# Optimization experiments

Measured on AMD Instinct MI355X. Metric: run time of the kernel, lower is better.

Reference implementation:

```python
import jax, jax.numpy as jnp
import numpy as np

HEAD_NUM = 8
EMB = 256
HEAD_SIZE = EMB // HEAD_NUM
POS_LEN = 128
ROPE_BASE = 100.0
LN_EPS = 1e-5
SOFTPICK_EPS = 1e-6


def _rope_tables():
    inv_freq = 1.0 / ROPE_BASE ** (jnp.arange(0, HEAD_SIZE, 2, dtype=jnp.float32) / HEAD_SIZE)
    t = jnp.arange(POS_LEN, dtype=jnp.float32)
    freqs = jnp.einsum('i,j->ij', t, inv_freq)          # [W, hs/2]
    freqs = jnp.concatenate([freqs, freqs], axis=-1)     # [W, hs]
    return jnp.sin(freqs), jnp.cos(freqs)


def _apply_rope(e, sin, cos):
    # e: [..., W, hs]; sin/cos: [W, hs]
    h = HEAD_SIZE // 2
    rot = jnp.concatenate([-e[..., h:], e[..., :h]], axis=-1)
    return e * cos + rot * sin


def _layernorm(x, g, b):
    mu = jnp.mean(x, axis=-1, keepdims=True)
    var = jnp.mean(jnp.square(x - mu), axis=-1, keepdims=True)
    return (x - mu) * jax.lax.rsqrt(var + LN_EPS) * g + b


def _softpick(x):
    m = jnp.max(x, axis=-1, keepdims=True)
    e = jnp.exp(x - m) - jnp.exp(-m)
    return jax.nn.relu(e) / (jnp.sum(jnp.abs(e), axis=-1, keepdims=True) + SOFTPICK_EPS)


def setup_inputs() -> dict:
    key = jax.random.key(0)
    ks = jax.random.split(key, 12)
    B, C, H, W = 4, EMB, 256, 128
    hn, hs = HEAD_NUM, HEAD_SIZE
    s = 0.02
    return {
        'left': jax.random.normal(ks[0], (B, C, H, W), jnp.float32),
        'right': jax.random.normal(ks[1], (B, C, H, W), jnp.float32),
        'qw': jax.random.normal(ks[2], (hn, hs, hs), jnp.float32) * s,   # grouped 1x1 conv weights
        'kw': jax.random.normal(ks[3], (hn, hs, hs), jnp.float32) * s,
        'vw': jax.random.normal(ks[4], (hn, hs, hs), jnp.float32) * s,
        'proj_w': jax.random.normal(ks[5], (C, C), jnp.float32) * s,
        'proj_b': jnp.zeros((C,), jnp.float32),
        'ln1_g': jnp.ones((C,), jnp.float32),
        'ln1_b': jnp.zeros((C,), jnp.float32),
        'ln2_g': jnp.ones((C,), jnp.float32),
        'ln2_b': jnp.zeros((C,), jnp.float32),
        'w1': jax.random.normal(ks[6], (C, 4 * C), jnp.float32) * s,
        'b1': jnp.zeros((4 * C,), jnp.float32),
        'w2': jax.random.normal(ks[7], (4 * C, C), jnp.float32) * s,
        'b2': jnp.zeros((C,), jnp.float32),
    }


def reference(left, right, qw, kw, vw, proj_w, proj_b,
              ln1_g, ln1_b, ln2_g, ln2_b, w1, b1, w2, b2):
    B, C, H, W = left.shape
    hn, hs = HEAD_NUM, HEAD_SIZE
    scale = hs ** -0.5
    sin, cos = _rope_tables()  # [W, hs]

    def grouped_proj(x, w):
        # grouped 1x1 conv -> per-head matmul; out [B, H, hn, W, hs]
        xr = x.reshape(B, hn, hs, H, W)
        return jnp.einsum('bgihw,goi->bhgwo', xr, w)

    q = _apply_rope(grouped_proj(left, qw), sin, cos)
    k = _apply_rope(grouped_proj(right, kw), sin, cos)
    v = grouped_proj(right, vw)

    att = _softpick(jnp.einsum('bhgqd,bhgkd->bhgqk', q, k) * scale)  # [B,H,hn,W,W]
    out = jnp.einsum('bhgqk,bhgkd->bhqgd', att, v).reshape(B, H, W, C)

    x1 = _layernorm(out @ proj_w + proj_b + jnp.transpose(left, (0, 2, 3, 1)), ln1_g, ln1_b)
    ffn = jax.nn.gelu(x1 @ w1 + b1, approximate=False) @ w2 + b2
    return _layernorm(ffn + x1, ln2_g, ln2_b)
```

## Files before the change

kernel.cpp:

```cpp
#include <hip/hip_runtime.h>
#include <hip/hip_bf16.h>

#define DEV __device__ __forceinline__

typedef __attribute__((ext_vector_type(8))) short bf16x8_t;
typedef __attribute__((ext_vector_type(4))) float f32x4_t;

constexpr int cB = 4, cC = 256, cH = 256, cW = 128, cHN = 8, cHS = 32;
constexpr int cM = cB * cH * cW;

DEV float bfu(unsigned int b16) { union { unsigned int u; float f; } v; v.u = b16 << 16; return v.f; }
DEV unsigned short f2bb(float f) { union { __hip_bfloat16 h; unsigned short u; } v; v.h = __float2bfloat16(f); return v.u; }
DEV unsigned int pk2(float a, float b) { return (unsigned)f2bb(a) | ((unsigned)f2bb(b) << 16); }

#define GLOAD_LDS16(g, l) \
  __builtin_amdgcn_global_load_lds((const __attribute__((address_space(1))) void*)(g), \
                                   (__attribute__((address_space(3))) void*)(l), 16, 0, 0)

DEV float gelu_fast(float v) {
  float ax = fabsf(v) * 0.7071067811865475f;
  float t = __builtin_amdgcn_rcpf(1.0f + 0.3275911f * ax);
  float poly = ((((1.061405429f * t - 1.453152027f) * t + 1.421413741f) * t
                 - 0.284496736f) * t + 0.254829592f) * t;
  float e = __expf(-ax * ax);
  float erfv = 1.0f - poly * e;
  float phi = 0.5f + 0.5f * copysignf(erfv, v);
  return v * phi;
}

__global__ __launch_bounds__(256) void transpose_bf16(const float* __restrict__ src,
                                                      __hip_bfloat16* __restrict__ dst,
                                                      int R, int Ccol) {
  int idx = blockIdx.x * 256 + threadIdx.x;
  if (idx < R * Ccol) {
    int r = idx / Ccol, c = idx - r * Ccol;
    dst[c * R + r] = __float2bfloat16(src[idx]);
  }
}

__global__ __launch_bounds__(256) void transpose_perm_fp8(const float* __restrict__ src,
                                                          unsigned char* __restrict__ dst,
                                                          int R, int Ccol) {
  int idx = blockIdx.x * 256 + threadIdx.x;
  if (idx < R * Ccol) {
    int r = idx / Ccol, c = idx - r * Ccol;
    int pk = (r & ~63) | ((r & 15) << 2) | ((r >> 4) & 3);
    int u = __builtin_amdgcn_cvt_pk_fp8_f32(src[idx] * 64.0f, 0.0f, 0, false);
    dst[(size_t)c * R + pk] = (unsigned char)(u & 0xff);
  }
}

__global__ __launch_bounds__(256) void rope_init(float2* __restrict__ tab) {
  int i = blockIdx.x * 256 + threadIdx.x;
  int w = i >> 4, c = i & 15;
  float inv = expf((float)c * -0.28782313662425572f);
  float ang = (float)w * inv;
  tab[i] = make_float2(sinf(ang), cosf(ang));
}

constexpr int XL_OFF = 0, XR_OFF = 10240, WQ_OFF = 20480, WK_OFF = 23040, WV_OFF = 25600;
constexpr int QS_OFF = 28160, KS_OFF = 38400, VT_OFF = 0, P_OFF = 10240;
constexpr int SMEM_BYTES = 48640;

__global__ __launch_bounds__(256) void attn_mfma(
    const float* __restrict__ left, const float* __restrict__ right,
    const float* __restrict__ qw, const float* __restrict__ kw, const float* __restrict__ vw,
    const float2* __restrict__ rope,
    __hip_bfloat16* __restrict__ att_out)
{
  __shared__ __align__(16) char smem[SMEM_BYTES];

  const int t = threadIdx.x;
  const int g = blockIdx.x & 7;
  const int h = (blockIdx.x >> 3) & 255;
  const int b = blockIdx.x >> 11;
  const size_t HW = (size_t)cH * cW;

  {
    const float* lb = left  + ((size_t)(b * cC + g * cHS) * cH + h) * cW;
    const float* rb = right + ((size_t)(b * cC + g * cHS) * cH + h) * cW;
    int w = t & 127, ih = (t >> 7) * 16;
    unsigned short* xlrow = (unsigned short*)(smem + XL_OFF) + w * 40 + ih;
    unsigned short* xrrow = (unsigned short*)(smem + XR_OFF) + w * 40 + ih;
#pragma unroll
    for (int i = 0; i < 16; i += 2) {
      float a0 = lb[(size_t)(ih + i) * HW + w], a1 = lb[(size_t)(ih + i + 1) * HW + w];
      *(unsigned int*)(xlrow + i) = pk2(a0, a1);
      float c0 = rb[(size_t)(ih + i) * HW + w], c1 = rb[(size_t)(ih + i + 1) * HW + w];
      *(unsigned int*)(xrrow + i) = pk2(c0, c1);
    }
    int o = t >> 3, i0 = (t & 7) * 4;
    {
      float4 v4 = *(const float4*)(qw + g * 1024 + t * 4);
      unsigned short* dst = (unsigned short*)(smem + WQ_OFF) + o * 40 + i0;
      *(unsigned int*)(dst) = pk2(v4.x, v4.y); *(unsigned int*)(dst + 2) = pk2(v4.z, v4.w);
    }
    {
      float4 v4 = *(const float4*)(kw + g * 1024 + t * 4);
      unsigned short* dst = (unsigned short*)(smem + WK_OFF) + o * 40 + i0;
      *(unsigned int*)(dst) = pk2(v4.x, v4.y); *(unsigned int*)(dst + 2) = pk2(v4.z, v4.w);
    }
    {
      float4 v4 = *(const float4*)(vw + g * 1024 + t * 4);
      unsigned short* dst = (unsigned short*)(smem + WV_OFF) + o * 40 + i0;
      *(unsigned int*)(dst) = pk2(v4.x, v4.y); *(unsigned int*)(dst + 2) = pk2(v4.z, v4.w);
    }
  }
  __syncthreads();

  const int lane = t & 63, wid = t >> 6;
  const int c = lane & 15, q4 = lane >> 4;
  const int wbase = wid * 32;
  const f32x4_t zero = {0.f, 0.f, 0.f, 0.f};

  bf16x8_t a_xl[2], a_xr[2];
#pragma unroll
  for (int sub = 0; sub < 2; ++sub) {
    a_xl[sub] = *(const bf16x8_t*)(smem + XL_OFF + (wbase + sub * 16 + c) * 80 + q4 * 16);
    a_xr[sub] = *(const bf16x8_t*)(smem + XR_OFF + (wbase + sub * 16 + c) * 80 + q4 * 16);
  }
  f32x4_t qacc[2][2], kacc[2][2];
#pragma unroll
  for (int ot = 0; ot < 2; ++ot) {
    bf16x8_t bq = *(const bf16x8_t*)(smem + WQ_OFF + (ot * 16 + c) * 80 + q4 * 16);
    bf16x8_t bk = *(const bf16x8_t*)(smem + WK_OFF + (ot * 16 + c) * 80 + q4 * 16);
#pragma unroll
    for (int sub = 0; sub < 2; ++sub) {
      qacc[sub][ot] = __builtin_amdgcn_mfma_f32_16x16x32_bf16(a_xl[sub], bq, zero, 0, 0, 0);
      kacc[sub][ot] = __builtin_amdgcn_mfma_f32_16x16x32_bf16(a_xr[sub], bk, zero, 0, 0, 0);
    }
  }
  {
    const float scale = 0.17677669529663687f;
    unsigned short* qsp = (unsigned short*)(smem + QS_OFF);
    unsigned short* ksp = (unsigned short*)(smem + KS_OFF);
#pragma unroll
    for (int sub = 0; sub < 2; ++sub)
#pragma unroll
      for (int r = 0; r < 4; ++r) {
        int w = wbase + sub * 16 + q4 * 4 + r;
        float2 sc = rope[w * 16 + c];
        float sn = sc.x, cs = sc.y;
        float q0 = qacc[sub][0][r], q1 = qacc[sub][1][r];
        qsp[w * 40 + c]      = f2bb((q0 * cs - q1 * sn) * scale);
        qsp[w * 40 + c + 16] = f2bb((q1 * cs + q0 * sn) * scale);
        float k0 = kacc[sub][0][r], k1 = kacc[sub][1][r];
        ksp[w * 40 + c]      = f2bb(k0 * cs - k1 * sn);
        ksp[w * 40 + c + 16] = f2bb(k1 * cs + k0 * sn);
      }
  }
  __syncthreads();

  {
    f32x4_t vacc[2][2];
#pragma unroll
    for (int dt = 0; dt < 2; ++dt) {
      bf16x8_t awv = *(const bf16x8_t*)(smem + WV_OFF + (dt * 16 + c) * 80 + q4 * 16);
#pragma unroll
      for (int sub = 0; sub < 2; ++sub)
        vacc[dt][sub] = __builtin_amdgcn_mfma_f32_16x16x32_bf16(awv, a_xr[sub], zero, 0, 0, 0);
    }
    unsigned short* vtp = (unsigned short*)(smem + VT_OFF);
#pragma unroll
    for (int dt = 0; dt < 2; ++dt)
#pragma unroll
      for (int r = 0; r < 4; ++r) {
        int d = dt * 16 + q4 * 4 + r;
        *(unsigned int*)(vtp + d * 136 + c * 8 + wid * 2) = pk2(vacc[dt][0][r], vacc[dt][1][r]);
      }
  }

  bf16x8_t aq0 = *(const bf16x8_t*)(smem + QS_OFF + (wbase + c) * 80 + q4 * 16);
  bf16x8_t aq1 = *(const bf16x8_t*)(smem + QS_OFF + (wbase + 16 + c) * 80 + q4 * 16);
  f32x4_t sac[2][8];
#pragma unroll
  for (int kt = 0; kt < 8; ++kt) {
    bf16x8_t bk = *(const bf16x8_t*)(smem + KS_OFF + (kt * 16 + c) * 80 + q4 * 16);
    sac[0][kt] = __builtin_amdgcn_mfma_f32_16x16x32_bf16(aq0, bk, zero, 0, 0, 0);
    sac[1][kt] = __builtin_amdgcn_mfma_f32_16x16x32_bf16(aq1, bk, zero, 0, 0, 0);
  }

  float dinv_[2][4];
#pragma unroll
  for (int sub = 0; sub < 2; ++sub)
#pragma unroll
    for (int r = 0; r < 4; ++r) {
      float m = sac[sub][0][r];
#pragma unroll
      for (int kt = 1; kt < 8; ++kt) m = fmaxf(m, sac[sub][kt][r]);
      m = fmaxf(m, __shfl_xor(m, 1));
      m = fmaxf(m, __shfl_xor(m, 2));
      m = fmaxf(m, __shfl_xor(m, 4));
      m = fmaxf(m, __shfl_xor(m, 8));
      float em = __expf(-m);
      float ss = 0.f;
#pragma unroll
      for (int kt = 0; kt < 8; ++kt) {
        float e = __expf(sac[sub][kt][r] - m) - em;
        sac[sub][kt][r] = fmaxf(e, 0.f);
        ss += fabsf(e);
      }
      ss += __shfl_xor(ss, 1);
      ss += __shfl_xor(ss, 2);
      ss += __shfl_xor(ss, 4);
      ss += __shfl_xor(ss, 8);
      dinv_[sub][r] = 1.0f / (ss + 1e-6f);
    }
  __syncthreads();

  {
    unsigned short* pp = (unsigned short*)(smem + P_OFF);
#pragma unroll
    for (int sub = 0; sub < 2; ++sub)
#pragma unroll
      for (int r = 0; r < 4; ++r) {
        int w = wbase + sub * 16 + q4 * 4 + r;
        float dv = dinv_[sub][r];
        uint4 u;
        u.x = pk2(sac[sub][0][r] * dv, sac[sub][1][r] * dv);
        u.y = pk2(sac[sub][2][r] * dv, sac[sub][3][r] * dv);
        u.z = pk2(sac[sub][4][r] * dv, sac[sub][5][r] * dv);
        u.w = pk2(sac[sub][6][r] * dv, sac[sub][7][r] * dv);
        *(uint4*)(pp + w * 136 + c * 8) = u;
      }
  }
  f32x4_t oacc[2][2] = {{zero, zero}, {zero, zero}};
#pragma unroll
  for (int ks = 0; ks < 4; ++ks) {
    bf16x8_t ap0 = *(const bf16x8_t*)(smem + P_OFF + (wbase + c) * 272 + ks * 64 + q4 * 16);
    bf16x8_t ap1 = *(const bf16x8_t*)(smem + P_OFF + (wbase + 16 + c) * 272 + ks * 64 + q4 * 16);
    bf16x8_t bv0 = *(const bf16x8_t*)(smem + VT_OFF + (c) * 272 + ks * 64 + q4 * 16);
    bf16x8_t bv1 = *(const bf16x8_t*)(smem + VT_OFF + (16 + c) * 272 + ks * 64 + q4 * 16);
    oacc[0][0] = __builtin_amdgcn_mfma_f32_16x16x32_bf16(ap0, bv0, oacc[0][0], 0, 0, 0);
    oacc[0][1] = __builtin_amdgcn_mfma_f32_16x16x32_bf16(ap0, bv1, oacc[0][1], 0, 0, 0);
    oacc[1][0] = __builtin_amdgcn_mfma_f32_16x16x32_bf16(ap1, bv0, oacc[1][0], 0, 0, 0);
    oacc[1][1] = __builtin_amdgcn_mfma_f32_16x16x32_bf16(ap1, bv1, oacc[1][1], 0, 0, 0);
  }
  {
    __hip_bfloat16* ob = att_out + ((size_t)(b * cH + h) * cW) * cC + g * cHS;
#pragma unroll
    for (int sub = 0; sub < 2; ++sub)
#pragma unroll
      for (int dt = 0; dt < 2; ++dt)
#pragma unroll
        for (int r = 0; r < 4; ++r) {
          int w = wbase + sub * 16 + q4 * 4 + r;
          ob[(size_t)w * cC + dt * 16 + c] = __float2bfloat16(oacc[sub][dt][r]);
        }
  }
}

__global__ __launch_bounds__(256) void ffn1_gemm(
    const __hip_bfloat16* __restrict__ A, const __hip_bfloat16* __restrict__ Bt,
    const float* __restrict__ bias, unsigned char* __restrict__ outb)
{
  constexpr int K = 256, N = 1024;
  __shared__ __align__(16) char smem[49152];
  const int t = threadIdx.x;
  const int id = blockIdx.x;
  const int slot = id >> 3;
  const int by = (id & 7) * 128 + (slot >> 3);
  const int bx = slot & 7;
  const int m0 = by * 128, n0 = bx * 128;
  const int lane = t & 63, wid = t >> 6;
  const int r16 = lane & 15, kq = lane >> 4;
  const int wr = (wid >> 1) * 64, wc = (wid & 1) * 64;

  f32x4_t acc[4][4];
#pragma unroll
  for (int fi = 0; fi < 4; ++fi)
#pragma unroll
    for (int fj = 0; fj < 4; ++fj) acc[fi][fj] = {0.f, 0.f, 0.f, 0.f};

  auto stage = [&](int buf, int k0) {
    char* As = smem + buf * 16384;
    char* Bs = As + 8192;
#pragma unroll
    for (int i = 0; i < 2; ++i) {
      int chunk = i * 4 + wid;
      int row = chunk * 16 + (lane >> 2);
      int sw = (((lane & 3) ^ ((row >> 1) & 3))) * 8;
      GLOAD_LDS16(A  + (size_t)(m0 + row) * K + k0 + sw, As + chunk * 1024);
      GLOAD_LDS16(Bt + (size_t)(n0 + row) * K + k0 + sw, Bs + chunk * 1024);
    }
  };

  constexpr int NK = K >> 5;
  stage(0, 0);
  stage(1, 32);
  for (int tt = 0; tt < NK; ++tt) {
    if (tt + 2 < NK) {
      stage((tt + 2) % 3, (tt + 2) << 5);
      asm volatile("s_waitcnt vmcnt(8)" ::: "memory");
    } else if (tt + 1 < NK) {
      asm volatile("s_waitcnt vmcnt(4)" ::: "memory");
    } else {
      asm volatile("s_waitcnt vmcnt(0)" ::: "memory");
    }
    __builtin_amdgcn_s_barrier();
    __builtin_amdgcn_sched_barrier(0);
    char* As = smem + (tt % 3) * 16384;
    char* Bs = As + 8192;
    bf16x8_t af[4], bf[4];
#pragma unroll
    for (int fi = 0; fi < 4; ++fi) {
      int rr = wr + fi * 16 + r16;
      af[fi] = *(const bf16x8_t*)(As + rr * 64 + ((kq ^ ((rr >> 1) & 3)) * 16));
    }
#pragma unroll
    for (int fj = 0; fj < 4; ++fj) {
      int rr = wc + fj * 16 + r16;
      bf[fj] = *(const bf16x8_t*)(Bs + rr * 64 + ((kq ^ ((rr >> 1) & 3)) * 16));
    }
#pragma unroll
    for (int fi = 0; fi < 4; ++fi)
#pragma unroll
      for (int fj = 0; fj < 4; ++fj)
        acc[fi][fj] = __builtin_amdgcn_mfma_f32_16x16x32_bf16(af[fi], bf[fj], acc[fi][fj], 0, 0, 0);
    __builtin_amdgcn_sched_barrier(0);
    __builtin_amdgcn_s_barrier();
  }

  float bv[4];
#pragma unroll
  for (int fj = 0; fj < 4; ++fj) bv[fj] = bias[n0 + wc + fj * 16 + r16];
  unsigned char* obase = outb + (size_t)(m0 + wr + kq * 4) * N + n0 + wc + r16 * 4;
#pragma unroll
  for (int fi = 0; fi < 4; ++fi)
#pragma unroll
    for (int r = 0; r < 4; ++r) {
      float v0 = gelu_fast(acc[fi][0][r] + bv[0]) * 64.0f;
      float v1 = gelu_fast(acc[fi][1][r] + bv[1]) * 64.0f;
      float v2 = gelu_fast(acc[fi][2][r] + bv[2]) * 64.0f;
      float v3 = gelu_fast(acc[fi][3][r] + bv[3]) * 64.0f;
      int u = __builtin_amdgcn_cvt_pk_fp8_f32(v0, v1, 0, false);
      u = __builtin_amdgcn_cvt_pk_fp8_f32(v2, v3, u, true);
      *(unsigned int*)(obase + (size_t)(fi * 16 + r) * N) = (unsigned)u;
    }
}

__global__ __launch_bounds__(256, 2) void proj_gemm_ln(
    const __hip_bfloat16* __restrict__ A, const __hip_bfloat16* __restrict__ Bt,
    const float* __restrict__ bias, const float* __restrict__ leftres,
    const float* __restrict__ g, const float* __restrict__ be,
    __hip_bfloat16* __restrict__ outp)
{
  constexpr int KK = 256;
  __shared__ __align__(16) char smem[73728];
  const int t = threadIdx.x, lane = t & 63, wid = t >> 6;
  const int c = lane & 15, q4 = lane >> 4;
  const int m0 = blockIdx.x * 128;
  const int wr = wid * 32;
  const f32x4_t zero = {0.f, 0.f, 0.f, 0.f};

  f32x4_t acc[2][16];
#pragma unroll
  for (int fi = 0; fi < 2; ++fi)
#pragma unroll
    for (int fj = 0; fj < 16; ++fj) acc[fi][fj] = zero;

  auto stage = [&](int buf, int k0) {
    char* As = smem + buf * 24576;
    char* Bs = As + 8192;
#pragma unroll
    for (int i = 0; i < 2; ++i) {
      int chunk = (wid * 2 + i);
      int row = chunk * 16 + (lane >> 2);
      int sw = (((lane & 3) ^ ((row >> 1) & 3))) * 8;
      GLOAD_LDS16(A + (size_t)(m0 + row) * KK + k0 + sw, As + chunk * 1024);
    }
#pragma unroll
    for (int i = 0; i < 4; ++i) {
      int chunk = (wid * 4 + i);
      int row = chunk * 16 + (lane >> 2);
      int sw = (((lane & 3) ^ ((row >> 1) & 3))) * 8;
      GLOAD_LDS16(Bt + (size_t)row * KK + k0 + sw, Bs + chunk * 1024);
    }
  };

  constexpr int NK = KK >> 5;
  stage(0, 0);
  stage(1, 32);
  for (int tt = 0; tt < NK; ++tt) {
    if (tt + 2 < NK) {
      stage((tt + 2) % 3, (tt + 2) << 5);
      asm volatile("s_waitcnt vmcnt(12)" ::: "memory");
    } else if (tt + 1 < NK) {
      asm volatile("s_waitcnt vmcnt(6)" ::: "memory");
    } else {
      asm volatile("s_waitcnt vmcnt(0)" ::: "memory");
    }
    __builtin_amdgcn_s_barrier();
    __builtin_amdgcn_sched_barrier(0);
    char* As = smem + (tt % 3) * 24576;
    char* Bs = As + 8192;
    int ra0 = wr + c, ra1 = wr + 16 + c;
    bf16x8_t af0 = *(const bf16x8_t*)(As + ra0 * 64 + ((q4 ^ ((ra0 >> 1) & 3)) * 16));
    bf16x8_t af1 = *(const bf16x8_t*)(As + ra1 * 64 + ((q4 ^ ((ra1 >> 1) & 3)) * 16));
#pragma unroll
    for (int fj = 0; fj < 16; ++fj) {
      int rb = fj * 16 + c;
      bf16x8_t bf = *(const bf16x8_t*)(Bs + rb * 64 + ((q4 ^ ((rb >> 1) & 3)) * 16));
      acc[0][fj] = __builtin_amdgcn_mfma_f32_16x16x32_bf16(af0, bf, acc[0][fj], 0, 0, 0);
      acc[1][fj] = __builtin_amdgcn_mfma_f32_16x16x32_bf16(af1, bf, acc[1][fj], 0, 0, 0);
    }
    __builtin_amdgcn_sched_barrier(0);
    __builtin_amdgcn_s_barrier();
  }

  {
    const int b_ = m0 >> 15, h_ = (m0 >> 7) & 255;
#pragma unroll
    for (int fj = 0; fj < 16; ++fj) {
      int n = fj * 16 + c;
      float bv = bias[n];
#pragma unroll
      for (int fi = 0; fi < 2; ++fi) {
        int w0 = wr + fi * 16 + q4 * 4;
        float4 lr = *(const float4*)(leftres + (((size_t)b_ * 256 + n) * 256 + h_) * 128 + w0);
        float la[4] = {lr.x, lr.y, lr.z, lr.w};
#pragma unroll
        for (int r = 0; r < 4; ++r) acc[fi][fj][r] += bv + la[r];
      }
    }
  }

  float mu[2][4], rs[2][4];
#pragma unroll
  for (int fi = 0; fi < 2; ++fi)
#pragma unroll
    for (int r = 0; r < 4; ++r) {
      float s = 0.f;
#pragma unroll
      for (int fj = 0; fj < 16; ++fj) s += acc[fi][fj][r];
      s += __shfl_xor(s, 1); s += __shfl_xor(s, 2); s += __shfl_xor(s, 4); s += __shfl_xor(s, 8);
      float m_ = s * (1.0f / 256.0f);
      float sq = 0.f;
#pragma unroll
      for (int fj = 0; fj < 16; ++fj) { float d = acc[fi][fj][r] - m_; sq += d * d; }
      sq += __shfl_xor(sq, 1); sq += __shfl_xor(sq, 2); sq += __shfl_xor(sq, 4); sq += __shfl_xor(sq, 8);
      mu[fi][r] = m_;
      rs[fi][r] = rsqrtf(sq * (1.0f / 256.0f) + 1e-5f);
    }
#pragma unroll
  for (int fj = 0; fj < 16; ++fj) {
    int n = fj * 16 + c;
    float gv = g[n], bev = be[n];
#pragma unroll
    for (int fi = 0; fi < 2; ++fi)
#pragma unroll
      for (int r = 0; r < 4; ++r) {
        int row = wr + fi * 16 + q4 * 4 + r;
        outp[(size_t)(m0 + row) * 256 + n] =
            __float2bfloat16((acc[fi][fj][r] - mu[fi][r]) * rs[fi][r] * gv + bev);
      }
  }
}

__global__ __launch_bounds__(256, 2) void ffn2_ln(
    const unsigned char* __restrict__ A, const unsigned char* __restrict__ Bt,
    const float* __restrict__ bias, const __hip_bfloat16* __restrict__ resbf,
    const float* __restrict__ g, const float* __restrict__ be,
    float* __restrict__ outp)
{
  constexpr int KK = 1024;
  __shared__ __align__(16) char smem[73728];
  const int t = threadIdx.x, lane = t & 63, wid = t >> 6;
  const int c = lane & 15, q4 = lane >> 4;
  const int m0 = blockIdx.x * 128;
  const int wr = wid * 32;
  const f32x4_t zero = {0.f, 0.f, 0.f, 0.f};

  f32x4_t acc[2][16];
#pragma unroll
  for (int fi = 0; fi < 2; ++fi)
#pragma unroll
    for (int fj = 0; fj < 16; ++fj) acc[fi][fj] = zero;

  auto stage = [&](int buf, int k0) {
    char* As = smem + buf * 24576;
    char* Bs = As + 8192;
#pragma unroll
    for (int i = 0; i < 2; ++i) {
      int chunk = (wid * 2 + i);
      int row = chunk * 16 + (lane >> 2);
      int sw = (((lane & 3) ^ ((row >> 1) & 3))) * 16;
      GLOAD_LDS16(A + (size_t)(m0 + row) * KK + k0 + sw, As + chunk * 1024);
    }
#pragma unroll
    for (int i = 0; i < 4; ++i) {
      int chunk = (wid * 4 + i);
      int row = chunk * 16 + (lane >> 2);
      int sw = (((lane & 3) ^ ((row >> 1) & 3))) * 16;
      GLOAD_LDS16(Bt + (size_t)row * KK + k0 + sw, Bs + chunk * 1024);
    }
  };

  constexpr int NK = 16;
  stage(0, 0);
  stage(1, 64);
  const int sl = (c >> 1) & 3;
  const int koff0 = ((((q4 >> 1)) ^ sl) << 4) | ((q4 & 1) << 3);
  const int koff1 = (((2 | (q4 >> 1)) ^ sl) << 4) | ((q4 & 1) << 3);
  for (int tt = 0; tt < NK; ++tt) {
    if (tt + 2 < NK) {
      stage((tt + 2) % 3, (tt + 2) << 6);
      asm volatile("s_waitcnt vmcnt(12)" ::: "memory");
    } else if (tt + 1 < NK) {
      asm volatile("s_waitcnt vmcnt(6)" ::: "memory");
    } else {
      asm volatile("s_waitcnt vmcnt(0)" ::: "memory");
    }
    __builtin_amdgcn_s_barrier();
    __builtin_amdgcn_sched_barrier(0);
    char* As = smem + (tt % 3) * 24576;
    char* Bs = As + 8192;
    const char* arow0 = As + (wr + c) * 64;
    const char* arow1 = As + (wr + 16 + c) * 64;
    long a00 = *(const long*)(arow0 + koff0);
    long a01 = *(const long*)(arow0 + koff1);
    long a10 = *(const long*)(arow1 + koff0);
    long a11 = *(const long*)(arow1 + koff1);
#pragma unroll
    for (int fj = 0; fj < 16; ++fj) {
      const char* brow = Bs + (fj * 16 + c) * 64;
      long b0 = *(const long*)(brow + koff0);
      long b1 = *(const long*)(brow + koff1);
      acc[0][fj] = __builtin_amdgcn_mfma_f32_16x16x32_fp8_fp8(a00, b0, acc[0][fj], 0, 0, 0);
      acc[0][fj] = __builtin_amdgcn_mfma_f32_16x16x32_fp8_fp8(a01, b1, acc[0][fj], 0, 0, 0);
      acc[1][fj] = __builtin_amdgcn_mfma_f32_16x16x32_fp8_fp8(a10, b0, acc[1][fj], 0, 0, 0);
      acc[1][fj] = __builtin_amdgcn_mfma_f32_16x16x32_fp8_fp8(a11, b1, acc[1][fj], 0, 0, 0);
    }
    __builtin_amdgcn_sched_barrier(0);
    __builtin_amdgcn_s_barrier();
  }

#pragma unroll
  for (int fj = 0; fj < 16; ++fj) {
    int n = fj * 16 + c;
    float bv = bias[n];
#pragma unroll
    for (int fi = 0; fi < 2; ++fi)
#pragma unroll
      for (int r = 0; r < 4; ++r) {
        int row = wr + fi * 16 + q4 * 4 + r;
        acc[fi][fj][r] = acc[fi][fj][r] * 0.000244140625f + bv +
                         __bfloat162float(resbf[(size_t)(m0 + row) * 256 + n]);
      }
  }

  float mu[2][4], rs[2][4];
#pragma unroll
  for (int fi = 0; fi < 2; ++fi)
#pragma unroll
    for (int r = 0; r < 4; ++r) {
      float s = 0.f;
#pragma unroll
      for (int fj = 0; fj < 16; ++fj) s += acc[fi][fj][r];
      s += __shfl_xor(s, 1); s += __shfl_xor(s, 2); s += __shfl_xor(s, 4); s += __shfl_xor(s, 8);
      float m_ = s * (1.0f / 256.0f);
      float sq = 0.f;
#pragma unroll
      for (int fj = 0; fj < 16; ++fj) { float d = acc[fi][fj][r] - m_; sq += d * d; }
      sq += __shfl_xor(sq, 1); sq += __shfl_xor(sq, 2); sq += __shfl_xor(sq, 4); sq += __shfl_xor(sq, 8);
      mu[fi][r] = m_;
      rs[fi][r] = rsqrtf(sq * (1.0f / 256.0f) + 1e-5f);
    }
#pragma unroll
  for (int fj = 0; fj < 16; ++fj) {
    int n = fj * 16 + c;
    float gv = g[n], bev = be[n];
#pragma unroll
    for (int fi = 0; fi < 2; ++fi)
#pragma unroll
      for (int r = 0; r < 4; ++r) {
        int row = wr + fi * 16 + q4 * 4 + r;
        outp[(size_t)(m0 + row) * 256 + n] =
            (acc[fi][fj][r] - mu[fi][r]) * rs[fi][r] * gv + bev;
      }
  }
}

extern "C" void kernel_launch(void* const* d_in, const int* in_sizes, int n_in,
                              void* d_out, int out_size, void* d_ws, size_t ws_size,
                              hipStream_t stream) {
  const float* left   = (const float*)d_in[0];
  const float* right  = (const float*)d_in[1];
  const float* qw     = (const float*)d_in[2];
  const float* kw     = (const float*)d_in[3];
  const float* vw     = (const float*)d_in[4];
  const float* proj_w = (const float*)d_in[5];
  const float* proj_b = (const float*)d_in[6];
  const float* ln1_g  = (const float*)d_in[7];
  const float* ln1_b  = (const float*)d_in[8];
  const float* ln2_g  = (const float*)d_in[9];
  const float* ln2_b  = (const float*)d_in[10];
  const float* w1     = (const float*)d_in[11];
  const float* b1     = (const float*)d_in[12];
  const float* w2     = (const float*)d_in[13];
  const float* b2     = (const float*)d_in[14];

  char* ws = (char*)d_ws;
  __hip_bfloat16* att_out = (__hip_bfloat16*)ws;
  __hip_bfloat16* x1      = (__hip_bfloat16*)(ws + 67108864);
  unsigned char*  hidden  = (unsigned char*)(ws + 134217728);
  float2*         rope    = (float2*)(ws + 134217728);
  __hip_bfloat16* pwT     = (__hip_bfloat16*)(ws + 402653184);
  __hip_bfloat16* w1T     = pwT + 65536;
  unsigned char*  w2T     = (unsigned char*)(w1T + 262144);

  transpose_bf16<<<256, 256, 0, stream>>>(proj_w, pwT, 256, 256);
  transpose_bf16<<<1024, 256, 0, stream>>>(w1, w1T, 256, 1024);
  transpose_perm_fp8<<<1024, 256, 0, stream>>>(w2, w2T, 1024, 256);
  rope_init<<<8, 256, 0, stream>>>(rope);

  attn_mfma<<<cB * cH * cHN, 256, 0, stream>>>(left, right, qw, kw, vw, rope, att_out);

  proj_gemm_ln<<<cM / 128, 256, 0, stream>>>(att_out, pwT, proj_b, left, ln1_g, ln1_b, x1);
  ffn1_gemm<<<8192, 256, 0, stream>>>(x1, w1T, b1, hidden);
  ffn2_ln<<<cM / 128, 256, 0, stream>>>(hidden, w2T, b2, x1, ln2_g, ln2_b, (float*)d_out);
}
```

Before: 406.4 us.

## Widen FFN1 GEMM tile to 128x256 with 16-byte FP8 stores and matching w2 permutation

```diff
diff --git a/kernel.cpp b/kernel.cpp
--- a/kernel.cpp
+++ b/kernel.cpp
@@ -44,7 +44,7 @@
   int idx = blockIdx.x * 256 + threadIdx.x;
   if (idx < R * Ccol) {
     int r = idx / Ccol, c = idx - r * Ccol;
-    int pk = (r & ~63) | ((r & 15) << 2) | ((r >> 4) & 3);
+    int pk = (r & ~255) | ((r & 15) << 4) | ((r >> 4) & 15);
     int u = __builtin_amdgcn_cvt_pk_fp8_f32(src[idx] * 64.0f, 0.0f, 0, false);
     dst[(size_t)c * R + pk] = (unsigned char)(u & 0xff);
   }
@@ -248,95 +248,6 @@
           ob[(size_t)w * cC + dt * 16 + c] = __float2bfloat16(oacc[sub][dt][r]);
         }
   }
-}
-
-__global__ __launch_bounds__(256) void ffn1_gemm(
-    const __hip_bfloat16* __restrict__ A, const __hip_bfloat16* __restrict__ Bt,
-    const float* __restrict__ bias, unsigned char* __restrict__ outb)
-{
-  constexpr int K = 256, N = 1024;
-  __shared__ __align__(16) char smem[49152];
-  const int t = threadIdx.x;
-  const int id = blockIdx.x;
-  const int slot = id >> 3;
-  const int by = (id & 7) * 128 + (slot >> 3);
-  const int bx = slot & 7;
-  const int m0 = by * 128, n0 = bx * 128;
-  const int lane = t & 63, wid = t >> 6;
-  const int r16 = lane & 15, kq = lane >> 4;
-  const int wr = (wid >> 1) * 64, wc = (wid & 1) * 64;
-
-  f32x4_t acc[4][4];
-#pragma unroll
-  for (int fi = 0; fi < 4; ++fi)
-#pragma unroll
-    for (int fj = 0; fj < 4; ++fj) acc[fi][fj] = {0.f, 0.f, 0.f, 0.f};
-
-  auto stage = [&](int buf, int k0) {
-    char* As = smem + buf * 16384;
-    char* Bs = As + 8192;
-#pragma unroll
-    for (int i = 0; i < 2; ++i) {
-      int chunk = i * 4 + wid;
-      int row = chunk * 16 + (lane >> 2);
-      int sw = (((lane & 3) ^ ((row >> 1) & 3))) * 8;
-      GLOAD_LDS16(A  + (size_t)(m0 + row) * K + k0 + sw, As + chunk * 1024);
-      GLOAD_LDS16(Bt + (size_t)(n0 + row) * K + k0 + sw, Bs + chunk * 1024);
-    }
-  };
-
-  constexpr int NK = K >> 5;
-  stage(0, 0);
-  stage(1, 32);
-  for (int tt = 0; tt < NK; ++tt) {
-    if (tt + 2 < NK) {
-      stage((tt + 2) % 3, (tt + 2) << 5);
-      asm volatile("s_waitcnt vmcnt(8)" ::: "memory");
-    } else if (tt + 1 < NK) {
-      asm volatile("s_waitcnt vmcnt(4)" ::: "memory");
-    } else {
-      asm volatile("s_waitcnt vmcnt(0)" ::: "memory");
-    }
-    __builtin_amdgcn_s_barrier();
-    __builtin_amdgcn_sched_barrier(0);
-    char* As = smem + (tt % 3) * 16384;
-    char* Bs = As + 8192;
-    bf16x8_t af[4], bf[4];
-#pragma unroll
-    for (int fi = 0; fi < 4; ++fi) {
-      int rr = wr + fi * 16 + r16;
-      af[fi] = *(const bf16x8_t*)(As + rr * 64 + ((kq ^ ((rr >> 1) & 3)) * 16));
-    }
-#pragma unroll
-    for (int fj = 0; fj < 4; ++fj) {
-      int rr = wc + fj * 16 + r16;
-      bf[fj] = *(const bf16x8_t*)(Bs + rr * 64 + ((kq ^ ((rr >> 1) & 3)) * 16));
-    }
-#pragma unroll
-    for (int fi = 0; fi < 4; ++fi)
-#pragma unroll
-      for (int fj = 0; fj < 4; ++fj)
-        acc[fi][fj] = __builtin_amdgcn_mfma_f32_16x16x32_bf16(af[fi], bf[fj], acc[fi][fj], 0, 0, 0);
-    __builtin_amdgcn_sched_barrier(0);
-    __builtin_amdgcn_s_barrier();
-  }
-
-  float bv[4];
-#pragma unroll
-  for (int fj = 0; fj < 4; ++fj) bv[fj] = bias[n0 + wc + fj * 16 + r16];
-  unsigned char* obase = outb + (size_t)(m0 + wr + kq * 4) * N + n0 + wc + r16 * 4;
-#pragma unroll
-  for (int fi = 0; fi < 4; ++fi)
-#pragma unroll
-    for (int r = 0; r < 4; ++r) {
-      float v0 = gelu_fast(acc[fi][0][r] + bv[0]) * 64.0f;
-      float v1 = gelu_fast(acc[fi][1][r] + bv[1]) * 64.0f;
-      float v2 = gelu_fast(acc[fi][2][r] + bv[2]) * 64.0f;
-      float v3 = gelu_fast(acc[fi][3][r] + bv[3]) * 64.0f;
-      int u = __builtin_amdgcn_cvt_pk_fp8_f32(v0, v1, 0, false);
-      u = __builtin_amdgcn_cvt_pk_fp8_f32(v2, v3, u, true);
-      *(unsigned int*)(obase + (size_t)(fi * 16 + r) * N) = (unsigned)u;
-    }
 }
 
 __global__ __launch_bounds__(256, 2) void proj_gemm_ln(
@@ -455,6 +366,100 @@
             __float2bfloat16((acc[fi][fj][r] - mu[fi][r]) * rs[fi][r] * gv + bev);
       }
   }
+}
+
+__global__ __launch_bounds__(256, 2) void ffn1_wide(
+    const __hip_bfloat16* __restrict__ A, const __hip_bfloat16* __restrict__ Bt,
+    const float* __restrict__ bias, unsigned char* __restrict__ outb)
+{
+  constexpr int KK = 256, N = 1024;
+  __shared__ __align__(16) char smem[73728];
+  const int t = threadIdx.x, lane = t & 63, wid = t >> 6;
+  const int c = lane & 15, q4 = lane >> 4;
+  const int mb = blockIdx.x & 1023, nc = blockIdx.x >> 10;
+  const int m0 = mb * 128, n0 = nc * 256;
+  const int wr = wid * 32;
+  const f32x4_t zero = {0.f, 0.f, 0.f, 0.f};
+
+  f32x4_t acc[2][16];
+#pragma unroll
+  for (int fi = 0; fi < 2; ++fi)
+#pragma unroll
+    for (int fj = 0; fj < 16; ++fj) acc[fi][fj] = zero;
+
+  const __hip_bfloat16* Bbase = Bt + (size_t)n0 * KK;
+
+  auto stage = [&](int buf, int k0) {
+    char* As = smem + buf * 24576;
+    char* Bs = As + 8192;
+#pragma unroll
+    for (int i = 0; i < 2; ++i) {
+      int chunk = (wid * 2 + i);
+      int row = chunk * 16 + (lane >> 2);
+      int sw = (((lane & 3) ^ ((row >> 1) & 3))) * 8;
+      GLOAD_LDS16(A + (size_t)(m0 + row) * KK + k0 + sw, As + chunk * 1024);
+    }
+#pragma unroll
+    for (int i = 0; i < 4; ++i) {
+      int chunk = (wid * 4 + i);
+      int row = chunk * 16 + (lane >> 2);
+      int sw = (((lane & 3) ^ ((row >> 1) & 3))) * 8;
+      GLOAD_LDS16(Bbase + (size_t)row * KK + k0 + sw, Bs + chunk * 1024);
+    }
+  };
+
+  constexpr int NK = KK >> 5;
+  stage(0, 0);
+  stage(1, 32);
+  for (int tt = 0; tt < NK; ++tt) {
+    if (tt + 2 < NK) {
+      stage((tt + 2) % 3, (tt + 2) << 5);
+      asm volatile("s_waitcnt vmcnt(12)" ::: "memory");
+    } else if (tt + 1 < NK) {
+      asm volatile("s_waitcnt vmcnt(6)" ::: "memory");
+    } else {
+      asm volatile("s_waitcnt vmcnt(0)" ::: "memory");
+    }
+    __builtin_amdgcn_s_barrier();
+    __builtin_amdgcn_sched_barrier(0);
+    char* As = smem + (tt % 3) * 24576;
+    char* Bs = As + 8192;
+    int ra0 = wr + c, ra1 = wr + 16 + c;
+    bf16x8_t af0 = *(const bf16x8_t*)(As + ra0 * 64 + ((q4 ^ ((ra0 >> 1) & 3)) * 16));
+    bf16x8_t af1 = *(const bf16x8_t*)(As + ra1 * 64 + ((q4 ^ ((ra1 >> 1) & 3)) * 16));
+#pragma unroll
+    for (int fj = 0; fj < 16; ++fj) {
+      int rb = fj * 16 + c;
+      bf16x8_t bf = *(const bf16x8_t*)(Bs + rb * 64 + ((q4 ^ ((rb >> 1) & 3)) * 16));
+      acc[0][fj] = __builtin_amdgcn_mfma_f32_16x16x32_bf16(af0, bf, acc[0][fj], 0, 0, 0);
+      acc[1][fj] = __builtin_amdgcn_mfma_f32_16x16x32_bf16(af1, bf, acc[1][fj], 0, 0, 0);
+    }
+    __builtin_amdgcn_sched_barrier(0);
+    __builtin_amdgcn_s_barrier();
+  }
+
+  float bv[16];
+#pragma unroll
+  for (int fj = 0; fj < 16; ++fj) bv[fj] = bias[n0 + fj * 16 + c];
+  unsigned char* obase = outb + (size_t)(m0 + wr + q4 * 4) * N + n0 + c * 16;
+#pragma unroll
+  for (int fi = 0; fi < 2; ++fi)
+#pragma unroll
+    for (int r = 0; r < 4; ++r) {
+      uint4 u;
+      unsigned int* up = (unsigned int*)&u;
+#pragma unroll
+      for (int p = 0; p < 4; ++p) {
+        float v0 = gelu_fast(acc[fi][4 * p + 0][r] + bv[4 * p + 0]) * 64.0f;
+        float v1 = gelu_fast(acc[fi][4 * p + 1][r] + bv[4 * p + 1]) * 64.0f;
+        float v2 = gelu_fast(acc[fi][4 * p + 2][r] + bv[4 * p + 2]) * 64.0f;
+        float v3 = gelu_fast(acc[fi][4 * p + 3][r] + bv[4 * p + 3]) * 64.0f;
+        int w = __builtin_amdgcn_cvt_pk_fp8_f32(v0, v1, 0, false);
+        w = __builtin_amdgcn_cvt_pk_fp8_f32(v2, v3, w, true);
+        up[p] = (unsigned)w;
+      }
+      *(uint4*)(obase + (size_t)(fi * 16 + r) * N) = u;
+    }
 }
 
 __global__ __launch_bounds__(256, 2) void ffn2_ln(
@@ -604,7 +609,7 @@
   __hip_bfloat16* att_out = (__hip_bfloat16*)ws;
   __hip_bfloat16* x1      = (__hip_bfloat16*)(ws + 67108864);
   unsigned char*  hidden  = (unsigned char*)(ws + 134217728);
-  float2*         rope    = (float2*)(ws + 134217728);
+  float2*         rope    = (float2*)(ws + 301989888);
   __hip_bfloat16* pwT     = (__hip_bfloat16*)(ws + 402653184);
   __hip_bfloat16* w1T     = pwT + 65536;
   unsigned char*  w2T     = (unsigned char*)(w1T + 262144);
@@ -617,6 +622,6 @@
   attn_mfma<<<cB * cH * cHN, 256, 0, stream>>>(left, right, qw, kw, vw, rope, att_out);
 
   proj_gemm_ln<<<cM / 128, 256, 0, stream>>>(att_out, pwT, proj_b, left, ln1_g, ln1_b, x1);
-  ffn1_gemm<<<8192, 256, 0, stream>>>(x1, w1T, b1, hidden);
+  ffn1_wide<<<4096, 256, 0, stream>>>(x1, w1T, b1, hidden);
   ffn2_ln<<<cM / 128, 256, 0, stream>>>(hidden, w2T, b2, x1, ln2_g, ln2_b, (float*)d_out);
 }
```

Result: no change. 411.7 us (+1.3%).

## Load attention inputs straight to registers and use FP8 for PV matmul

Applied to the files above, without the earlier changes.

```diff
diff --git a/kernel.cpp b/kernel.cpp
--- a/kernel.cpp
+++ b/kernel.cpp
@@ -58,11 +58,11 @@
   tab[i] = make_float2(sinf(ang), cosf(ang));
 }
 
-constexpr int XL_OFF = 0, XR_OFF = 10240, WQ_OFF = 20480, WK_OFF = 23040, WV_OFF = 25600;
-constexpr int QS_OFF = 28160, KS_OFF = 38400, VT_OFF = 0, P_OFF = 10240;
-constexpr int SMEM_BYTES = 48640;
-
-__global__ __launch_bounds__(256) void attn_mfma(
+constexpr int WQ_OFF = 0, WK_OFF = 2560, WV_OFF = 5120, QS_OFF = 7680, KS_OFF = 17920;
+constexpr int VT_OFF = 28160, P_OFF = 0;
+constexpr int SMEM_BYTES = 32512;
+
+__global__ __launch_bounds__(256, 4) void attn_mfma(
     const float* __restrict__ left, const float* __restrict__ right,
     const float* __restrict__ qw, const float* __restrict__ kw, const float* __restrict__ vw,
     const float2* __restrict__ rope,
@@ -76,19 +76,35 @@
   const int b = blockIdx.x >> 11;
   const size_t HW = (size_t)cH * cW;
 
+  const int lane = t & 63, wid = t >> 6;
+  const int c = lane & 15, q4 = lane >> 4;
+  const int wbase = wid * 32;
+  const f32x4_t zero = {0.f, 0.f, 0.f, 0.f};
+
+  const float* lb = left  + ((size_t)(b * cC + g * cHS) * cH + h) * cW;
+  const float* rb = right + ((size_t)(b * cC + g * cHS) * cH + h) * cW;
+
+  bf16x8_t a_xl[2], a_xr[2];
+#pragma unroll
+  for (int sub = 0; sub < 2; ++sub) {
+    int w = wbase + sub * 16 + c;
+    float xl[8], xr[8];
+#pragma unroll
+    for (int e = 0; e < 8; ++e) {
+      xl[e] = lb[(size_t)(q4 * 8 + e) * HW + w];
+      xr[e] = rb[(size_t)(q4 * 8 + e) * HW + w];
+    }
+    union { bf16x8_t v; unsigned int u[4]; } ul, ur;
+#pragma unroll
+    for (int p = 0; p < 4; ++p) {
+      ul.u[p] = pk2(xl[2 * p], xl[2 * p + 1]);
+      ur.u[p] = pk2(xr[2 * p], xr[2 * p + 1]);
+    }
+    a_xl[sub] = ul.v;
+    a_xr[sub] = ur.v;
+  }
+
   {
-    const float* lb = left  + ((size_t)(b * cC + g * cHS) * cH + h) * cW;
-    const float* rb = right + ((size_t)(b * cC + g * cHS) * cH + h) * cW;
-    int w = t & 127, ih = (t >> 7) * 16;
-    unsigned short* xlrow = (unsigned short*)(smem + XL_OFF) + w * 40 + ih;
-    unsigned short* xrrow = (unsigned short*)(smem + XR_OFF) + w * 40 + ih;
-#pragma unroll
-    for (int i = 0; i < 16; i += 2) {
-      float a0 = lb[(size_t)(ih + i) * HW + w], a1 = lb[(size_t)(ih + i + 1) * HW + w];
-      *(unsigned int*)(xlrow + i) = pk2(a0, a1);
-      float c0 = rb[(size_t)(ih + i) * HW + w], c1 = rb[(size_t)(ih + i + 1) * HW + w];
-      *(unsigned int*)(xrrow + i) = pk2(c0, c1);
-    }
     int o = t >> 3, i0 = (t & 7) * 4;
     {
       float4 v4 = *(const float4*)(qw + g * 1024 + t * 4);
@@ -108,17 +124,6 @@
   }
   __syncthreads();
 
-  const int lane = t & 63, wid = t >> 6;
-  const int c = lane & 15, q4 = lane >> 4;
-  const int wbase = wid * 32;
-  const f32x4_t zero = {0.f, 0.f, 0.f, 0.f};
-
-  bf16x8_t a_xl[2], a_xr[2];
-#pragma unroll
-  for (int sub = 0; sub < 2; ++sub) {
-    a_xl[sub] = *(const bf16x8_t*)(smem + XL_OFF + (wbase + sub * 16 + c) * 80 + q4 * 16);
-    a_xr[sub] = *(const bf16x8_t*)(smem + XR_OFF + (wbase + sub * 16 + c) * 80 + q4 * 16);
-  }
   f32x4_t qacc[2][2], kacc[2][2];
 #pragma unroll
   for (int ot = 0; ot < 2; ++ot) {
@@ -160,13 +165,15 @@
       for (int sub = 0; sub < 2; ++sub)
         vacc[dt][sub] = __builtin_amdgcn_mfma_f32_16x16x32_bf16(awv, a_xr[sub], zero, 0, 0, 0);
     }
-    unsigned short* vtp = (unsigned short*)(smem + VT_OFF);
+    unsigned char* vtp = (unsigned char*)(smem + VT_OFF);
 #pragma unroll
     for (int dt = 0; dt < 2; ++dt)
 #pragma unroll
       for (int r = 0; r < 4; ++r) {
         int d = dt * 16 + q4 * 4 + r;
-        *(unsigned int*)(vtp + d * 136 + c * 8 + wid * 2) = pk2(vacc[dt][0][r], vacc[dt][1][r]);
+        int u = __builtin_amdgcn_cvt_pk_fp8_f32(vacc[dt][0][r] * 16.0f,
+                                                vacc[dt][1][r] * 16.0f, 0, false);
+        *(unsigned short*)(vtp + d * 136 + c * 8 + wid * 2) = (unsigned short)(u & 0xffff);
       }
   }
 
@@ -209,32 +216,33 @@
   __syncthreads();
 
   {
-    unsigned short* pp = (unsigned short*)(smem + P_OFF);
+    unsigned char* pp = (unsigned char*)(smem + P_OFF);
 #pragma unroll
     for (int sub = 0; sub < 2; ++sub)
 #pragma unroll
       for (int r = 0; r < 4; ++r) {
         int w = wbase + sub * 16 + q4 * 4 + r;
-        float dv = dinv_[sub][r];
-        uint4 u;
-        u.x = pk2(sac[sub][0][r] * dv, sac[sub][1][r] * dv);
-        u.y = pk2(sac[sub][2][r] * dv, sac[sub][3][r] * dv);
-        u.z = pk2(sac[sub][4][r] * dv, sac[sub][5][r] * dv);
-        u.w = pk2(sac[sub][6][r] * dv, sac[sub][7][r] * dv);
-        *(uint4*)(pp + w * 136 + c * 8) = u;
-      }
-  }
+        float s16 = dinv_[sub][r] * 16.0f;
+        int u0 = __builtin_amdgcn_cvt_pk_fp8_f32(sac[sub][0][r] * s16, sac[sub][1][r] * s16, 0, false);
+        u0 = __builtin_amdgcn_cvt_pk_fp8_f32(sac[sub][2][r] * s16, sac[sub][3][r] * s16, u0, true);
+        int u1 = __builtin_amdgcn_cvt_pk_fp8_f32(sac[sub][4][r] * s16, sac[sub][5][r] * s16, 0, false);
+        u1 = __builtin_amdgcn_cvt_pk_fp8_f32(sac[sub][6][r] * s16, sac[sub][7][r] * s16, u1, true);
+        uint2 u; u.x = (unsigned)u0; u.y = (unsigned)u1;
+        *(uint2*)(pp + w * 136 + c * 8) = u;
+      }
+  }
+
   f32x4_t oacc[2][2] = {{zero, zero}, {zero, zero}};
 #pragma unroll
   for (int ks = 0; ks < 4; ++ks) {
-    bf16x8_t ap0 = *(const bf16x8_t*)(smem + P_OFF + (wbase + c) * 272 + ks * 64 + q4 * 16);
-    bf16x8_t ap1 = *(const bf16x8_t*)(smem + P_OFF + (wbase + 16 + c) * 272 + ks * 64 + q4 * 16);
-    bf16x8_t bv0 = *(const bf16x8_t*)(smem + VT_OFF + (c) * 272 + ks * 64 + q4 * 16);
-    bf16x8_t bv1 = *(const bf16x8_t*)(smem + VT_OFF + (16 + c) * 272 + ks * 64 + q4 * 16);
-    oacc[0][0] = __builtin_amdgcn_mfma_f32_16x16x32_bf16(ap0, bv0, oacc[0][0], 0, 0, 0);
-    oacc[0][1] = __builtin_amdgcn_mfma_f32_16x16x32_bf16(ap0, bv1, oacc[0][1], 0, 0, 0);
-    oacc[1][0] = __builtin_amdgcn_mfma_f32_16x16x32_bf16(ap1, bv0, oacc[1][0], 0, 0, 0);
-    oacc[1][1] = __builtin_amdgcn_mfma_f32_16x16x32_bf16(ap1, bv1, oacc[1][1], 0, 0, 0);
+    long ap0 = *(const long*)(smem + P_OFF + (wbase + c) * 136 + ks * 32 + q4 * 8);
+    long ap1 = *(const long*)(smem + P_OFF + (wbase + 16 + c) * 136 + ks * 32 + q4 * 8);
+    long bv0 = *(const long*)(smem + VT_OFF + (c) * 136 + ks * 32 + q4 * 8);
+    long bv1 = *(const long*)(smem + VT_OFF + (16 + c) * 136 + ks * 32 + q4 * 8);
+    oacc[0][0] = __builtin_amdgcn_mfma_f32_16x16x32_fp8_fp8(ap0, bv0, oacc[0][0], 0, 0, 0);
+    oacc[0][1] = __builtin_amdgcn_mfma_f32_16x16x32_fp8_fp8(ap0, bv1, oacc[0][1], 0, 0, 0);
+    oacc[1][0] = __builtin_amdgcn_mfma_f32_16x16x32_fp8_fp8(ap1, bv0, oacc[1][0], 0, 0, 0);
+    oacc[1][1] = __builtin_amdgcn_mfma_f32_16x16x32_fp8_fp8(ap1, bv1, oacc[1][1], 0, 0, 0);
   }
   {
     __hip_bfloat16* ob = att_out + ((size_t)(b * cH + h) * cW) * cC + g * cHS;
@@ -245,7 +253,7 @@
 #pragma unroll
         for (int r = 0; r < 4; ++r) {
           int w = wbase + sub * 16 + q4 * 4 + r;
-          ob[(size_t)w * cC + dt * 16 + c] = __float2bfloat16(oacc[sub][dt][r]);
+          ob[(size_t)w * cC + dt * 16 + c] = __float2bfloat16(oacc[sub][dt][r] * 0.00390625f);
         }
   }
 }
@@ -604,7 +612,7 @@
   __hip_bfloat16* att_out = (__hip_bfloat16*)ws;
   __hip_bfloat16* x1      = (__hip_bfloat16*)(ws + 67108864);
   unsigned char*  hidden  = (unsigned char*)(ws + 134217728);
-  float2*         rope    = (float2*)(ws + 134217728);
+  float2*         rope    = (float2*)(ws + 301989888);
   __hip_bfloat16* pwT     = (__hip_bfloat16*)(ws + 402653184);
   __hip_bfloat16* w1T     = pwT + 65536;
   unsigned char*  w2T     = (unsigned char*)(w1T + 262144);
```

New measurement: 424.2 us. +4.4%, slower.
